# Performance work log

Hardware: AMD Instinct MI355X
Metric: run time of the kernel (lower is better)

The kernel has to match this reference:

```python
import jax, jax.numpy as jnp
import numpy as np

D_MODEL = 1024
N_LAYERS = 2
D_STATE = 16
D_CONV = 4
D_INNER = 2 * D_MODEL          # mamba expand=2
DT_RANK = 64                   # ceil(d_model/16)
EPS = 1e-5


def rmsnorm(x, w, eps=EPS):
    return x * jax.lax.rsqrt(jnp.mean(x * x, axis=-1, keepdims=True) + eps) * w


def silu(x):
    return x * jax.nn.sigmoid(x)


def selective_scan(u, dt, A, B, C, Dp):
    # u, dt: (b,l,d)  A: (d,n)  B,C: (b,l,n)  Dp: (d,)
    b, l, d = u.shape
    n = A.shape[1]

    def step(h, inp):
        u_t, dt_t, B_t, C_t = inp          # (b,d),(b,d),(b,n),(b,n)
        dA = jnp.exp(dt_t[..., None] * A)  # (b,d,n)
        h = dA * h + (dt_t * u_t)[..., None] * B_t[:, None, :]
        y = jnp.einsum('bdn,bn->bd', h, C_t)
        return h, y

    h0 = jnp.zeros((b, d, n), u.dtype)
    xs = (u.transpose(1, 0, 2), dt.transpose(1, 0, 2),
          B.transpose(1, 0, 2), C.transpose(1, 0, 2))
    _, ys = jax.lax.scan(step, h0, xs)
    return ys.transpose(1, 0, 2) + u * Dp


def mamba_mixer(x, in_w, conv_w, conv_b, xp_w, dt_w, dt_b, A_log, Dp, out_w):
    b, l, _ = x.shape
    xz = jnp.einsum('bld,ed->ble', x, in_w)        # (b,l,2*d_inner)
    xi, z = jnp.split(xz, 2, axis=-1)
    # depthwise causal conv1d, kernel D_CONV
    xp = jnp.pad(xi, ((0, 0), (D_CONV - 1, 0), (0, 0)))
    xc = conv_b + sum(xp[:, k:k + l, :] * conv_w[:, k] for k in range(D_CONV))
    xc = silu(xc)
    dbc = jnp.einsum('bld,ed->ble', xc, xp_w)      # (b,l,dt_rank+2n)
    dt_low = dbc[..., :DT_RANK]
    Bm = dbc[..., DT_RANK:DT_RANK + D_STATE]
    Cm = dbc[..., DT_RANK + D_STATE:]
    dt = jax.nn.softplus(jnp.einsum('blr,dr->bld', dt_low, dt_w) + dt_b)
    A = -jnp.exp(A_log)
    y = selective_scan(xc, dt, A, Bm, Cm, Dp)
    y = y * silu(z)
    return jnp.einsum('bld,od->blo', y, out_w)


def setup_inputs() -> dict:
    key = jax.random.key(0)
    ks = jax.random.split(key, 8)
    s = 0.02
    hidden_states = jax.random.normal(ks[0], (1, 2048, D_MODEL), jnp.float32)
    norm_w = jnp.ones((N_LAYERS, D_MODEL), jnp.float32)
    in_proj_w = jax.random.normal(ks[1], (N_LAYERS, 2 * D_INNER, D_MODEL), jnp.float32) * s
    conv_w = jax.random.normal(ks[2], (N_LAYERS, D_INNER, D_CONV), jnp.float32) * 0.2
    conv_b = jnp.zeros((N_LAYERS, D_INNER), jnp.float32)
    x_proj_w = jax.random.normal(ks[3], (N_LAYERS, DT_RANK + 2 * D_STATE, D_INNER), jnp.float32) * s
    dt_proj_w = jax.random.normal(ks[4], (N_LAYERS, D_INNER, DT_RANK), jnp.float32) * (DT_RANK ** -0.5)
    # softplus^{-1}(0.01) ~= -4.6 (mamba dt bias init regime)
    dt_proj_b = jnp.full((N_LAYERS, D_INNER), -4.6, jnp.float32) + \
        jax.random.normal(ks[5], (N_LAYERS, D_INNER), jnp.float32) * 0.1
    A_log = jnp.log(jnp.broadcast_to(
        jnp.arange(1, D_STATE + 1, dtype=jnp.float32), (N_LAYERS, D_INNER, D_STATE)))
    D_param = jnp.ones((N_LAYERS, D_INNER), jnp.float32)
    out_proj_w = jax.random.normal(ks[6], (N_LAYERS, D_MODEL, D_INNER), jnp.float32) * s
    norm_f_w = jnp.ones((D_MODEL,), jnp.float32)
    return {
        'hidden_states': hidden_states, 'norm_w': norm_w, 'in_proj_w': in_proj_w,
        'conv_w': conv_w, 'conv_b': conv_b, 'x_proj_w': x_proj_w,
        'dt_proj_w': dt_proj_w, 'dt_proj_b': dt_proj_b, 'A_log': A_log,
        'D_param': D_param, 'out_proj_w': out_proj_w, 'norm_f_w': norm_f_w,
    }


def reference(hidden_states, norm_w, in_proj_w, conv_w, conv_b, x_proj_w,
              dt_proj_w, dt_proj_b, A_log, D_param, out_proj_w, norm_f_w):
    h = hidden_states
    residual = None
    for i in range(N_LAYERS):
        # fused add + RMSNorm (prenorm): residual accumulates the stream
        residual = h if residual is None else h + residual
        hn = rmsnorm(residual, norm_w[i])
        h = mamba_mixer(hn, in_proj_w[i], conv_w[i], conv_b[i], x_proj_w[i],
                        dt_proj_w[i], dt_proj_b[i], A_log[i], D_param[i], out_proj_w[i])
    # final fused add + RMSNorm (prenorm=False)
    return rmsnorm(h + residual, norm_f_w)
```

## Files before the change

kernel.cpp:

```cpp
#include <hip/hip_runtime.h>
#include <math.h>

#define D_MODEL 1024
#define D_INNER 2048
#define DPROJ   96
#define DT_RANK 64
#define NSTATE  16
#define SEQ     2048
#define CL      16
#define NCH     (SEQ/CL)
#define SCAN_SEGS 4
#define SCAN_CPS  (NCH / SCAN_SEGS)
#define LOG2E   1.44269504088896340736f
#define TDC     ((size_t)SEQ * D_MODEL)

typedef unsigned short ushort_t;
typedef short v8s __attribute__((ext_vector_type(8)));
typedef unsigned short u8s __attribute__((ext_vector_type(8)));
typedef float v4f __attribute__((ext_vector_type(4)));
typedef __attribute__((address_space(3))) unsigned int as3_u32;
typedef __attribute__((address_space(1))) unsigned int as1_u32;

__device__ __forceinline__ float silu_f(float x) { return x / (1.f + expf(-x)); }

__device__ __forceinline__ ushort_t f2bf(float f) {
  union { float f; unsigned u; } x; x.f = f;
  unsigned r = x.u + 0x7fffu + ((x.u >> 16) & 1u);
  return (ushort_t)(r >> 16);
}
__device__ __forceinline__ float bf2f(ushort_t b) {
  union { unsigned u; float f; } x; x.u = ((unsigned)b) << 16; return x.f;
}

__device__ __forceinline__ void gl_lds16(const ushort_t* g, ushort_t* l) {
  __builtin_amdgcn_global_load_lds((const as1_u32*)g, (as3_u32*)l, 16, 0, 0);
}

__global__ __launch_bounds__(256) void addrms_kernel(
    const float* __restrict__ a, const ushort_t* __restrict__ p4,
    const float* __restrict__ b,
    const float* __restrict__ w, float* __restrict__ res_out,
    float* __restrict__ xnf, ushort_t* __restrict__ xnb) {
  int t = blockIdx.x;
  int tid = threadIdx.x;
  float v[4];
  float ss = 0.f;
#pragma unroll
  for (int j = 0; j < 4; ++j) {
    int dcol = tid + j * 256;
    size_t off = (size_t)t * D_MODEL + dcol;
    float x;
    if (p4) {
      x = bf2f(p4[off]) + bf2f(p4[off + TDC]) +
          bf2f(p4[off + 2 * TDC]) + bf2f(p4[off + 3 * TDC]);
    } else {
      x = a[off];
    }
    if (b) x += b[off];
    v[j] = x;
    ss += x * x;
  }
#pragma unroll
  for (int off = 32; off > 0; off >>= 1) ss += __shfl_down(ss, off);
  __shared__ float red[4];
  __shared__ float rmsv;
  int wid = tid >> 6, lane = tid & 63;
  if (lane == 0) red[wid] = ss;
  __syncthreads();
  if (tid == 0) {
    float s = red[0] + red[1] + red[2] + red[3];
    rmsv = rsqrtf(s / (float)D_MODEL + 1e-5f);
  }
  __syncthreads();
  float r = rmsv;
#pragma unroll
  for (int j = 0; j < 4; ++j) {
    int dcol = tid + j * 256;
    if (res_out) res_out[(size_t)t * D_MODEL + dcol] = v[j];
    float xn = v[j] * r * w[dcol];
    if (xnf) xnf[(size_t)t * D_MODEL + dcol] = xn;
    if (xnb) xnb[(size_t)t * D_MODEL + dcol] = f2bf(xn);
  }
}

__global__ __launch_bounds__(256) void f2bf_all_kernel(
    const float* __restrict__ s0, ushort_t* __restrict__ d0, int n0,
    const float* __restrict__ s1, ushort_t* __restrict__ d1, int n1,
    const float* __restrict__ s2, ushort_t* __restrict__ d2, int n2,
    const float* __restrict__ s3, ushort_t* __restrict__ d3, int n3) {
  int j = blockIdx.x * 256 + threadIdx.x;
  const float* s; ushort_t* d;
  if (j < n0) { s = s0; d = d0; }
  else {
    j -= n0;
    if (j < n1) { s = s1; d = d1; }
    else {
      j -= n1;
      if (j < n2) { s = s2; d = d2; }
      else {
        j -= n2;
        if (j >= n3) return;
        s = s3; d = d3;
      }
    }
  }
  float4 v = ((const float4*)s)[j];
  ushort4 o;
  o.x = f2bf(v.x); o.y = f2bf(v.y); o.z = f2bf(v.z); o.w = f2bf(v.w);
  ((ushort4*)d)[j] = o;
}

template <int SPLITK, bool CLAMPN, int EPI>
__global__ __launch_bounds__(256) void gemm_bt(
    const ushort_t* __restrict__ A, const ushort_t* __restrict__ B,
    void* __restrict__ Cv, const float* __restrict__ bias,
    const ushort_t* __restrict__ upack,
    int M, int N, int K, int lda, int ldb, int ldc) {
  __shared__ ushort_t As[2][128 * 32];
  __shared__ ushort_t Bs[2][128 * 32];
  int tid = threadIdx.x;

  int gx = gridDim.x, gy = gridDim.y;
  int nwg = gx * gy * gridDim.z;
  int phys = blockIdx.x + gx * (blockIdx.y + gy * blockIdx.z);
  int q = nwg >> 3, r = nwg & 7;
  int xcd = phys & 7, idx8 = phys >> 3;
  int lbid = (xcd < r ? xcd * (q + 1) : r * (q + 1) + (xcd - r) * q) + idx8;
  int bx = lbid % gx, by = (lbid / gx) % gy, bz = lbid / (gx * gy);

  int bm = by * 128;
  int bn = bx * 128;
  int kchunk = K / SPLITK;
  int k0 = bz * kchunk;
  int nk = kchunk / 32;

  int lane = tid & 63, wid = tid >> 6;
  int wr = wid >> 1, wc = wid & 1;
  int lr = lane & 15;
  int ko = (lane >> 4) * 8;

  int rs0 = wid * 16 + (lane >> 2);
  int segc = (lane & 3) * 8;

  auto stage = [&](int buf, int kt) {
#pragma unroll
    for (int s = 0; s < 2; ++s) {
      int r2 = s * 64 + rs0;
      int cc = kt + segc;
      gl_lds16(A + (size_t)(bm + r2) * lda + cc, &As[buf][s * 2048 + wid * 512]);
      int bc = bn + r2;
      if (CLAMPN) bc = min(bc, N - 1);
      gl_lds16(B + (size_t)bc * ldb + cc, &Bs[buf][s * 2048 + wid * 512]);
    }
  };

  v4f acc[4][4] = {};

  stage(0, k0);
  __syncthreads();
  int cur = 0;
  for (int it = 0; it < nk; ++it) {
    if (it + 1 < nk) stage(cur ^ 1, k0 + (it + 1) * 32);
    v8s a[4], b[4];
#pragma unroll
    for (int m = 0; m < 4; ++m)
      a[m] = *(const v8s*)&As[cur][(wr * 64 + m * 16 + lr) * 32 + ko];
#pragma unroll
    for (int n = 0; n < 4; ++n)
      b[n] = *(const v8s*)&Bs[cur][(wc * 64 + n * 16 + lr) * 32 + ko];
#pragma unroll
    for (int m = 0; m < 4; ++m)
#pragma unroll
      for (int n = 0; n < 4; ++n)
        acc[m][n] = __builtin_amdgcn_mfma_f32_16x16x32_bf16(a[m], b[n], acc[m][n], 0, 0, 0);
    __syncthreads();
    cur ^= 1;
  }

  float* Cf = (float*)Cv;
  ushort_t* Cb = (ushort_t*)Cv;
  unsigned* Cu = (unsigned*)Cv;
  size_t zoff = (SPLITK > 1) ? (size_t)bz * (size_t)M * (size_t)ldc : 0;

#pragma unroll
  for (int m = 0; m < 4; ++m) {
#pragma unroll
    for (int n = 0; n < 4; ++n) {
      int gc = bn + wc * 64 + n * 16 + lr;
      if (gc >= N) continue;
      int gr0 = bm + wr * 64 + m * 16 + (lane >> 4) * 4;
      float bv = (EPI == 1 || EPI == 3) ? bias[gc] : 0.f;
#pragma unroll
      for (int j = 0; j < 4; ++j) {
        float val = acc[m][n][j];
        size_t idx = zoff + (size_t)(gr0 + j) * ldc + gc;
        if (EPI == 0) {
          Cf[idx] = val;
        } else if (EPI == 1) {
          float x = val + bv;
          x = fmaxf(x, 0.f) + log1pf(expf(-fabsf(x)));
          Cb[idx] = f2bf(x);
        } else if (EPI == 2) {
          Cb[idx] = f2bf(val);
        } else {
          float x = val + bv;
          x = fmaxf(x, 0.f) + log1pf(expf(-fabsf(x)));
          Cu[idx] = (unsigned)f2bf(x) | ((unsigned)upack[idx] << 16);
        }
      }
    }
  }
}

__global__ __launch_bounds__(256) void reduceNb_kernel(
    const ushort_t* __restrict__ part, ushort_t* __restrict__ outb,
    int sz, int nparts) {
  int idx = blockIdx.x * 256 + threadIdx.x;
  if (idx >= sz) return;
  float s = 0.f;
  for (int p = 0; p < nparts; ++p) s += bf2f(part[idx + (size_t)p * sz]);
  outb[idx] = f2bf(s);
}

__global__ __launch_bounds__(256) void conv_silu_kernel(
    const ushort_t* __restrict__ xzb, const float* __restrict__ cw,
    const float* __restrict__ cb, ushort_t* __restrict__ xcb) {
  int idx = blockIdx.x * 256 + threadIdx.x;
  int tq = idx >> 9;
  int c = (idx & 511) * 4;
  int t0 = tq * 4;
  float4 cbv = *(const float4*)&cb[c];
  float4 wv[4];
#pragma unroll
  for (int i = 0; i < 4; ++i) wv[i] = *(const float4*)&cw[(c + i) * 4];
  float rows[7][4];
#pragma unroll
  for (int k = 0; k < 7; ++k) {
    int ts = t0 - 3 + k;
    if (ts < 0) {
      rows[k][0] = rows[k][1] = rows[k][2] = rows[k][3] = 0.f;
    } else {
      ushort4 x = *(const ushort4*)&xzb[(size_t)ts * 4096 + c];
      rows[k][0] = bf2f(x.x); rows[k][1] = bf2f(x.y);
      rows[k][2] = bf2f(x.z); rows[k][3] = bf2f(x.w);
    }
  }
#pragma unroll
  for (int j = 0; j < 4; ++j) {
    float acc[4] = {cbv.x, cbv.y, cbv.z, cbv.w};
#pragma unroll
    for (int k = 0; k < 4; ++k) {
#pragma unroll
      for (int i = 0; i < 4; ++i)
        acc[i] = fmaf(rows[j + k][i], ((const float*)&wv[i])[k], acc[i]);
    }
    ushort4 o;
    o.x = f2bf(silu_f(acc[0]));
    o.y = f2bf(silu_f(acc[1]));
    o.z = f2bf(silu_f(acc[2]));
    o.w = f2bf(silu_f(acc[3]));
    *(ushort4*)&xcb[(size_t)(t0 + j) * D_INNER + c] = o;
  }
}

__global__ __launch_bounds__(256) void scan_passA_kernel(
    const unsigned* __restrict__ dtu, const ushort_t* __restrict__ dbcb,
    const float* __restrict__ A_log,
    ushort_t* __restrict__ aprodb, ushort_t* __restrict__ hendb) {
  __shared__ float Bsh[CL][16];
  int c = blockIdx.x;
  int d = blockIdx.y * 256 + threadIdx.x;
  int t0 = c * CL;
  {
    int j = threadIdx.x;
    if (j < CL * 4) {
      int r = j >> 2, col = (j & 3) * 4;
      ushort4 v = *(const ushort4*)&dbcb[(size_t)(t0 + r) * DPROJ + DT_RANK + col];
      Bsh[r][col]     = bf2f(v.x);
      Bsh[r][col + 1] = bf2f(v.y);
      Bsh[r][col + 2] = bf2f(v.z);
      Bsh[r][col + 3] = bf2f(v.w);
    }
  }
  float Av[NSTATE], h[NSTATE], ap[NSTATE];
#pragma unroll
  for (int n = 0; n < NSTATE; ++n) {
    Av[n] = -expf(A_log[(size_t)d * NSTATE + n]) * LOG2E;
    h[n] = 0.f;
    ap[n] = 1.f;
  }
  __syncthreads();
#pragma unroll 2
  for (int tt = 0; tt < CL; ++tt) {
    unsigned p = dtu[(size_t)(t0 + tt) * D_INNER + d];
    float dtv = bf2f((ushort_t)(p & 0xffffu));
    float uv  = bf2f((ushort_t)(p >> 16));
    float du = dtv * uv;
#pragma unroll
    for (int n = 0; n < NSTATE; ++n) {
      float dA = exp2f(dtv * Av[n]);
      h[n] = fmaf(dA, h[n], du * Bsh[tt][n]);
      ap[n] *= dA;
    }
  }
  size_t base = ((size_t)c * D_INNER + d) * NSTATE;
  u8s oa, ob, ha, hb;
#pragma unroll
  for (int n = 0; n < 8; ++n) {
    oa[n] = f2bf(ap[n]);     ob[n] = f2bf(ap[n + 8]);
    ha[n] = f2bf(h[n]);      hb[n] = f2bf(h[n + 8]);
  }
  *(u8s*)&aprodb[base] = oa;     *(u8s*)&aprodb[base + 8] = ob;
  *(u8s*)&hendb[base]  = ha;     *(u8s*)&hendb[base + 8]  = hb;
}

__global__ __launch_bounds__(256) void scan_passB_kernel(
    const ushort_t* __restrict__ aprodb, ushort_t* __restrict__ hendb) {
  int tid = threadIdx.x;
  int lane = tid & 63;
  int wave = tid >> 6;
  int seg = lane >> 4;
  int chain = blockIdx.x * 64 + wave * 16 + (lane & 15);
  const size_t stride = (size_t)D_INNER * NSTATE;
  float a[SCAN_CPS], e[SCAN_CPS];
  float P = 1.f, E = 0.f;
  int c0 = seg * SCAN_CPS;
#pragma unroll
  for (int j = 0; j < SCAN_CPS; ++j) {
    a[j] = bf2f(aprodb[(size_t)(c0 + j) * stride + chain]);
    e[j] = bf2f(hendb[(size_t)(c0 + j) * stride + chain]);
    E = fmaf(a[j], E, e[j]);
    P *= a[j];
  }
#pragma unroll
  for (int dstep = 1; dstep < SCAN_SEGS; dstep <<= 1) {
    float Pp = __shfl_up(P, dstep * 16);
    float Ep = __shfl_up(E, dstep * 16);
    if (seg >= dstep) { E = fmaf(P, Ep, E); P *= Pp; }
  }
  float Ex = __shfl_up(E, 16);
  if (seg == 0) Ex = 0.f;
  float h = Ex;
#pragma unroll
  for (int j = 0; j < SCAN_CPS; ++j) {
    hendb[(size_t)(c0 + j) * stride + chain] = f2bf(h);
    h = fmaf(a[j], h, e[j]);
  }
}

__global__ __launch_bounds__(256) void scan_passC_kernel(
    const unsigned* __restrict__ dtu, const ushort_t* __restrict__ dbcb,
    const float* __restrict__ A_log, const float* __restrict__ Dp,
    const ushort_t* __restrict__ xzb, const ushort_t* __restrict__ hinb,
    ushort_t* __restrict__ yb) {
  __shared__ float BCsh[CL][32];
  int c = blockIdx.x;
  int d = blockIdx.y * 256 + threadIdx.x;
  int t0 = c * CL;
  {
    int j = threadIdx.x;
    if (j < CL * 8) {
      int r = j >> 3, col = (j & 7) * 4;
      ushort4 v = *(const ushort4*)&dbcb[(size_t)(t0 + r) * DPROJ + DT_RANK + col];
      BCsh[r][col]     = bf2f(v.x);
      BCsh[r][col + 1] = bf2f(v.y);
      BCsh[r][col + 2] = bf2f(v.z);
      BCsh[r][col + 3] = bf2f(v.w);
    }
  }
  float Av[NSTATE], h[NSTATE];
  size_t base = ((size_t)c * D_INNER + d) * NSTATE;
  u8s h0 = *(const u8s*)&hinb[base];
  u8s h1 = *(const u8s*)&hinb[base + 8];
#pragma unroll
  for (int n = 0; n < NSTATE; ++n) {
    Av[n] = -expf(A_log[(size_t)d * NSTATE + n]) * LOG2E;
    h[n] = (n < 8) ? bf2f(h0[n & 7]) : bf2f(h1[n & 7]);
  }
  float Dv = Dp[d];
  __syncthreads();
#pragma unroll 2
  for (int tt = 0; tt < CL; ++tt) {
    unsigned p = dtu[(size_t)(t0 + tt) * D_INNER + d];
    float dtv = bf2f((ushort_t)(p & 0xffffu));
    float uv  = bf2f((ushort_t)(p >> 16));
    float du = dtv * uv;
    float yv = 0.f;
#pragma unroll
    for (int n = 0; n < NSTATE; ++n) {
      float dA = exp2f(dtv * Av[n]);
      h[n] = fmaf(dA, h[n], du * BCsh[tt][n]);
      yv = fmaf(h[n], BCsh[tt][16 + n], yv);
    }
    float zv = bf2f(xzb[(size_t)(t0 + tt) * 4096 + D_INNER + d]);
    yb[(size_t)(t0 + tt) * D_INNER + d] = f2bf((yv + uv * Dv) * silu_f(zv));
  }
}

extern "C" void kernel_launch(void* const* d_in, const int* in_sizes, int n_in,
                              void* d_out, int out_size, void* d_ws, size_t ws_size,
                              hipStream_t stream) {
  const float* h_in   = (const float*)d_in[0];
  const float* norm_w = (const float*)d_in[1];
  const float* in_w   = (const float*)d_in[2];
  const float* conv_w = (const float*)d_in[3];
  const float* conv_b = (const float*)d_in[4];
  const float* xp_w   = (const float*)d_in[5];
  const float* dt_w   = (const float*)d_in[6];
  const float* dt_b   = (const float*)d_in[7];
  const float* A_log  = (const float*)d_in[8];
  const float* Dp     = (const float*)d_in[9];
  const float* out_w  = (const float*)d_in[10];
  const float* normf  = (const float*)d_in[11];
  float* out = (float*)d_out;

  float* ws = (float*)d_ws;
  const size_t TD = (size_t)SEQ * D_MODEL;
  const size_t TI = (size_t)SEQ * D_INNER;
  const size_t ST = (size_t)NCH * D_INNER * NSTATE;
  const size_t DB = (size_t)SEQ * DPROJ;
  const size_t INW = (size_t)2 * D_INNER * D_MODEL;
  const size_t XPW = (size_t)DPROJ * D_INNER;
  const size_t DTW = (size_t)D_INNER * DT_RANK;
  const size_t OUW = (size_t)D_MODEL * D_INNER;

  float* res = ws; ws += TD;
  ushort_t* pkb = (ushort_t*)ws; ws += 2 * TD;
  unsigned* dtu = (unsigned*)ws; ws += TI;
  ushort_t* us = (ushort_t*)ws;
  ushort_t* aprodb = us;  us += ST;
  ushort_t* hendb  = us;  us += ST;
  ushort_t* hnb  = us;    us += TD;
  ushort_t* xzb  = us;    us += 2 * TI;
  ushort_t* xcb  = us;    us += TI;
  ushort_t* ybf  = us;    us += TI;
  ushort_t* dbcb = us;    us += DB;
  ushort_t* inwb = us;    us += 2 * INW;
  ushort_t* xpwb = us;    us += 2 * XPW;
  ushort_t* dtwb = us;    us += 2 * DTW;
  ushort_t* ouwb = us;    us += 2 * OUW;

  {
    int n0 = (int)(2 * INW / 4), n1 = (int)(2 * XPW / 4);
    int n2 = (int)(2 * DTW / 4), n3 = (int)(2 * OUW / 4);
    int tot = n0 + n1 + n2 + n3;
    f2bf_all_kernel<<<(tot + 255) / 256, 256, 0, stream>>>(
        in_w, inwb, n0, xp_w, xpwb, n1, dt_w, dtwb, n2, out_w, ouwb, n3);
  }

  for (int i = 0; i < 2; ++i) {
    addrms_kernel<<<SEQ, 256, 0, stream>>>(
        h_in, i == 0 ? nullptr : pkb,
        i == 0 ? nullptr : res,
        norm_w + (size_t)i * D_MODEL, res, nullptr, hnb);
    gemm_bt<1, false, 2><<<dim3(32, 16, 1), 256, 0, stream>>>(
        hnb, inwb + (size_t)i * INW, xzb, nullptr, nullptr,
        SEQ, 2 * D_INNER, D_MODEL, D_MODEL, D_MODEL, 2 * D_INNER);
    conv_silu_kernel<<<(int)(TI / 16 / 256), 256, 0, stream>>>(
        xzb, conv_w + (size_t)i * D_INNER * 4, conv_b + (size_t)i * D_INNER, xcb);
    gemm_bt<16, true, 2><<<dim3(1, 16, 16), 256, 0, stream>>>(
        xcb, xpwb + (size_t)i * XPW, pkb, nullptr, nullptr,
        SEQ, DPROJ, D_INNER, D_INNER, D_INNER, DPROJ);
    reduceNb_kernel<<<(DB + 255) / 256, 256, 0, stream>>>(pkb, dbcb, (int)DB, 16);
    gemm_bt<1, false, 3><<<dim3(16, 16, 1), 256, 0, stream>>>(
        dbcb, dtwb + (size_t)i * DTW, dtu, dt_b + (size_t)i * D_INNER, xcb,
        SEQ, D_INNER, DT_RANK, DPROJ, DT_RANK, D_INNER);
    scan_passA_kernel<<<dim3(NCH, D_INNER / 256), 256, 0, stream>>>(
        dtu, dbcb, A_log + (size_t)i * D_INNER * NSTATE, aprodb, hendb);
    scan_passB_kernel<<<(D_INNER * NSTATE) / 64, 256, 0, stream>>>(aprodb, hendb);
    scan_passC_kernel<<<dim3(NCH, D_INNER / 256), 256, 0, stream>>>(
        dtu, dbcb, A_log + (size_t)i * D_INNER * NSTATE,
        Dp + (size_t)i * D_INNER, xzb, hendb, ybf);
    gemm_bt<4, false, 2><<<dim3(8, 16, 4), 256, 0, stream>>>(
        ybf, ouwb + (size_t)i * OUW, pkb, nullptr, nullptr,
        SEQ, D_MODEL, D_INNER, D_INNER, D_INNER, D_MODEL);
  }
  addrms_kernel<<<SEQ, 256, 0, stream>>>(
      h_in, pkb, res, normf, nullptr, out, nullptr);
}
```

Measured before the change: 349.1 us.

## Fuse depthwise conv+SiLU into the split-K x_proj GEMM via shared-memory A tile

Replaces the separate conv_silu kernel and the split-K x_proj GEMM with one kernel. Each block computes the causal conv and SiLU for its 128x128 tile straight into LDS, still writes xc to global for later stages, then runs MFMA against double-buffered x_proj weight tiles and writes per-split partials. This removes one launch and the global re-read of xc by the GEMM. The cost is a serial conv prologue before the MFMA loop and only 256 blocks for the whole fused stage.

```diff
diff --git a/kernel.cpp b/kernel.cpp
--- a/kernel.cpp
+++ b/kernel.cpp
@@ -212,6 +212,117 @@
   }
 }
 
+__global__ __launch_bounds__(256) void convxproj_kernel(
+    const ushort_t* __restrict__ xzb, const float* __restrict__ cw,
+    const float* __restrict__ cb, const ushort_t* __restrict__ Bw,
+    ushort_t* __restrict__ xcb, ushort_t* __restrict__ pkb) {
+  __shared__ ushort_t As[128][136];
+  __shared__ ushort_t Bs[2][128 * 32];
+  int tid = threadIdx.x;
+  int bm = blockIdx.y * 128;
+  int c0s = blockIdx.z * 128;
+  int k0 = c0s;
+
+  {
+    int quad = tid & 31;
+    int tg = tid >> 5;
+    int cc = c0s + quad * 4;
+    int tbase = bm + tg * 16;
+    float4 cbv = *(const float4*)&cb[cc];
+    float4 wv[4];
+#pragma unroll
+    for (int i = 0; i < 4; ++i) wv[i] = *(const float4*)&cw[(cc + i) * 4];
+    float rw[4][4];
+#pragma unroll
+    for (int p = 0; p < 3; ++p) {
+      int ts = tbase - 3 + p;
+      if (ts < 0) {
+        rw[p][0] = rw[p][1] = rw[p][2] = rw[p][3] = 0.f;
+      } else {
+        ushort4 x = *(const ushort4*)&xzb[(size_t)ts * 4096 + cc];
+        rw[p][0] = bf2f(x.x); rw[p][1] = bf2f(x.y);
+        rw[p][2] = bf2f(x.z); rw[p][3] = bf2f(x.w);
+      }
+    }
+#pragma unroll
+    for (int j = 0; j < 16; ++j) {
+      int t = tbase + j;
+      {
+        ushort4 x = *(const ushort4*)&xzb[(size_t)t * 4096 + cc];
+        rw[(3 + j) & 3][0] = bf2f(x.x); rw[(3 + j) & 3][1] = bf2f(x.y);
+        rw[(3 + j) & 3][2] = bf2f(x.z); rw[(3 + j) & 3][3] = bf2f(x.w);
+      }
+      float acc[4] = {cbv.x, cbv.y, cbv.z, cbv.w};
+#pragma unroll
+      for (int k = 0; k < 4; ++k) {
+#pragma unroll
+        for (int i = 0; i < 4; ++i)
+          acc[i] = fmaf(rw[(j + k) & 3][i], ((const float*)&wv[i])[k], acc[i]);
+      }
+      ushort4 o;
+      o.x = f2bf(silu_f(acc[0]));
+      o.y = f2bf(silu_f(acc[1]));
+      o.z = f2bf(silu_f(acc[2]));
+      o.w = f2bf(silu_f(acc[3]));
+      *(ushort4*)&As[tg * 16 + j][quad * 4] = o;
+      *(ushort4*)&xcb[(size_t)t * D_INNER + cc] = o;
+    }
+  }
+
+  int lane = tid & 63, wid = tid >> 6;
+  int wr = wid >> 1, wc = wid & 1;
+  int lr = lane & 15;
+  int ko = (lane >> 4) * 8;
+  int rs0 = wid * 16 + (lane >> 2);
+  int segc = (lane & 3) * 8;
+
+  auto stageB = [&](int buf, int it) {
+#pragma unroll
+    for (int s = 0; s < 2; ++s) {
+      int r2 = s * 64 + rs0;
+      int bc = min(r2, DPROJ - 1);
+      int cc2 = k0 + it * 32 + segc;
+      gl_lds16(Bw + (size_t)bc * D_INNER + cc2, &Bs[buf][s * 2048 + wid * 512]);
+    }
+  };
+
+  v4f acc[4][4] = {};
+  stageB(0, 0);
+  __syncthreads();
+  int cur = 0;
+  for (int it = 0; it < 4; ++it) {
+    if (it + 1 < 4) stageB(cur ^ 1, it + 1);
+    v8s a[4], b[4];
+#pragma unroll
+    for (int m = 0; m < 4; ++m)
+      a[m] = *(const v8s*)&As[wr * 64 + m * 16 + lr][it * 32 + ko];
+#pragma unroll
+    for (int n = 0; n < 4; ++n)
+      b[n] = *(const v8s*)&Bs[cur][(wc * 64 + n * 16 + lr) * 32 + ko];
+#pragma unroll
+    for (int m = 0; m < 4; ++m)
+#pragma unroll
+      for (int n = 0; n < 4; ++n)
+        acc[m][n] = __builtin_amdgcn_mfma_f32_16x16x32_bf16(a[m], b[n], acc[m][n], 0, 0, 0);
+    __syncthreads();
+    cur ^= 1;
+  }
+
+  size_t zoff = (size_t)blockIdx.z * (size_t)SEQ * DPROJ;
+#pragma unroll
+  for (int m = 0; m < 4; ++m) {
+#pragma unroll
+    for (int n = 0; n < 4; ++n) {
+      int gc = wc * 64 + n * 16 + lr;
+      if (gc >= DPROJ) continue;
+      int gr0 = bm + wr * 64 + m * 16 + (lane >> 4) * 4;
+#pragma unroll
+      for (int j = 0; j < 4; ++j)
+        pkb[zoff + (size_t)(gr0 + j) * DPROJ + gc] = f2bf(acc[m][n][j]);
+    }
+  }
+}
+
 __global__ __launch_bounds__(256) void reduceNb_kernel(
     const ushort_t* __restrict__ part, ushort_t* __restrict__ outb,
     int sz, int nparts) {
@@ -220,47 +331,6 @@
   float s = 0.f;
   for (int p = 0; p < nparts; ++p) s += bf2f(part[idx + (size_t)p * sz]);
   outb[idx] = f2bf(s);
-}
-
-__global__ __launch_bounds__(256) void conv_silu_kernel(
-    const ushort_t* __restrict__ xzb, const float* __restrict__ cw,
-    const float* __restrict__ cb, ushort_t* __restrict__ xcb) {
-  int idx = blockIdx.x * 256 + threadIdx.x;
-  int tq = idx >> 9;
-  int c = (idx & 511) * 4;
-  int t0 = tq * 4;
-  float4 cbv = *(const float4*)&cb[c];
-  float4 wv[4];
-#pragma unroll
-  for (int i = 0; i < 4; ++i) wv[i] = *(const float4*)&cw[(c + i) * 4];
-  float rows[7][4];
-#pragma unroll
-  for (int k = 0; k < 7; ++k) {
-    int ts = t0 - 3 + k;
-    if (ts < 0) {
-      rows[k][0] = rows[k][1] = rows[k][2] = rows[k][3] = 0.f;
-    } else {
-      ushort4 x = *(const ushort4*)&xzb[(size_t)ts * 4096 + c];
-      rows[k][0] = bf2f(x.x); rows[k][1] = bf2f(x.y);
-      rows[k][2] = bf2f(x.z); rows[k][3] = bf2f(x.w);
-    }
-  }
-#pragma unroll
-  for (int j = 0; j < 4; ++j) {
-    float acc[4] = {cbv.x, cbv.y, cbv.z, cbv.w};
-#pragma unroll
-    for (int k = 0; k < 4; ++k) {
-#pragma unroll
-      for (int i = 0; i < 4; ++i)
-        acc[i] = fmaf(rows[j + k][i], ((const float*)&wv[i])[k], acc[i]);
-    }
-    ushort4 o;
-    o.x = f2bf(silu_f(acc[0]));
-    o.y = f2bf(silu_f(acc[1]));
-    o.z = f2bf(silu_f(acc[2]));
-    o.w = f2bf(silu_f(acc[3]));
-    *(ushort4*)&xcb[(size_t)(t0 + j) * D_INNER + c] = o;
-  }
 }
 
 __global__ __launch_bounds__(256) void scan_passA_kernel(
@@ -456,11 +526,9 @@
     gemm_bt<1, false, 2><<<dim3(32, 16, 1), 256, 0, stream>>>(
         hnb, inwb + (size_t)i * INW, xzb, nullptr, nullptr,
         SEQ, 2 * D_INNER, D_MODEL, D_MODEL, D_MODEL, 2 * D_INNER);
-    conv_silu_kernel<<<(int)(TI / 16 / 256), 256, 0, stream>>>(
-        xzb, conv_w + (size_t)i * D_INNER * 4, conv_b + (size_t)i * D_INNER, xcb);
-    gemm_bt<16, true, 2><<<dim3(1, 16, 16), 256, 0, stream>>>(
-        xcb, xpwb + (size_t)i * XPW, pkb, nullptr, nullptr,
-        SEQ, DPROJ, D_INNER, D_INNER, D_INNER, DPROJ);
+    convxproj_kernel<<<dim3(1, 16, 16), 256, 0, stream>>>(
+        xzb, conv_w + (size_t)i * D_INNER * 4, conv_b + (size_t)i * D_INNER,
+        xpwb + (size_t)i * XPW, xcb, pkb);
     reduceNb_kernel<<<(DB + 255) / 256, 256, 0, stream>>>(pkb, dbcb, (int)DB, 16);
     gemm_bt<1, false, 3><<<dim3(16, 16, 1), 256, 0, stream>>>(
         dbcb, dtwb + (size_t)i * DTW, dtu, dt_b + (size_t)i * D_INNER, xcb,
```

Measured after the change: 340.3 us. 1.03x faster.
